# Kernel tuning notes

Hardware: AMD Instinct MI355X
Metric: run time of the kernel (lower is better)

The kernel has to match this reference:

```python
import jax, jax.numpy as jnp
import numpy as np
import math

B, S, D = 4, 2048, 1024
H, DH = 16, 64  # num_heads, head dim (hardcoded 64 in module)


def setup_inputs() -> dict:
    key = jax.random.key(0)
    ks = jax.random.split(key, 5)
    scale = 0.02
    return {
        "x": jax.random.normal(ks[0], (B, S, D), dtype=jnp.float32),
        "W_Q": jax.random.normal(ks[1], (D, H * DH), dtype=jnp.float32) * scale,
        "W_K": jax.random.normal(ks[2], (D, H * DH), dtype=jnp.float32) * scale,
        "W_V": jax.random.normal(ks[3], (D, H * DH), dtype=jnp.float32) * scale,
        "W_O": jax.random.normal(ks[4], (H * DH, D), dtype=jnp.float32) * scale,
        "ln_gamma": jnp.ones((D,), dtype=jnp.float32),
        "ln_beta": jnp.zeros((D,), dtype=jnp.float32),
    }


def reference(x, W_Q, W_K, W_V, W_O, ln_gamma, ln_beta):
    # QKV projections (bias=False Linear: x @ W)
    q = (x @ W_Q).reshape(B, S, H, DH).transpose(0, 2, 1, 3)  # [B,H,S,DH]
    k = (x @ W_K).reshape(B, S, H, DH).transpose(0, 2, 1, 3)
    v = (x @ W_V).reshape(B, S, H, DH).transpose(0, 2, 1, 3)

    # scaled scores with causal mask (upper triangle, diag=1 -> -1e7)
    scores = jnp.einsum("bhsd,bhtd->bhst", q, k) / math.sqrt(DH)  # [B,H,S,S]
    causal = jnp.triu(jnp.ones((S, S), dtype=bool), k=1)
    scores = jnp.where(causal, jnp.float32(-1e7), scores)
    attn = jax.nn.softmax(scores, axis=-1)
    ctx = jnp.einsum("bhst,bhtd->bhsd", attn, v)  # [B,H,S,DH]

    # merge heads, output proj, residual, LayerNorm
    out = ctx.transpose(0, 2, 1, 3).reshape(B, S, H * DH) @ W_O + x
    mu = jnp.mean(out, axis=-1, keepdims=True)
    var = jnp.mean((out - mu) ** 2, axis=-1, keepdims=True)
    out = (out - mu) * jax.lax.rsqrt(var + 1e-5) * ln_gamma + ln_beta
    return out
```

## Files before the change

### kernel.cpp

```cpp
#include <hip/hip_runtime.h>
#include <hip/hip_bf16.h>
#include <cstdint>
#include <cstddef>

#define S_ 2048
#define D_ 1024
#define H_ 16
#define DH_ 64
#define M_ 8192

using bf16 = __bf16;
using bf16x4 = __attribute__((ext_vector_type(4))) __bf16;
using bf16x8 = __attribute__((ext_vector_type(8))) __bf16;
using f32x4 = __attribute__((ext_vector_type(4))) float;
using s16x4 = __attribute__((ext_vector_type(4))) short;

__device__ __forceinline__ void g2lds16(const bf16* g, bf16* l) {
  __builtin_amdgcn_global_load_lds(
      (const __attribute__((address_space(1))) void*)g,
      (__attribute__((address_space(3))) void*)l, 16, 0, 0);
}

__device__ __forceinline__ f32x4 mfma16(bf16x4 a, bf16x4 b, f32x4 c) {
#if __has_builtin(__builtin_amdgcn_mfma_f32_16x16x16_bf16)
  return __builtin_amdgcn_mfma_f32_16x16x16_bf16(a, b, c, 0, 0, 0);
#elif __has_builtin(__builtin_amdgcn_mfma_f32_16x16x16bf16_1k)
  return __builtin_amdgcn_mfma_f32_16x16x16bf16_1k(
      __builtin_bit_cast(s16x4, a), __builtin_bit_cast(s16x4, b), c, 0, 0, 0);
#else
  f32x4 d;
  asm("v_mfma_f32_16x16x16_bf16 %0, %1, %2, %3"
      : "=v"(d)
      : "v"(a), "v"(b), "v"(c));
  return d;
#endif
}

__global__ __launch_bounds__(256) void cvt_all_kernel(
    const float* __restrict__ x, const float* __restrict__ w0,
    const float* __restrict__ w1, const float* __restrict__ w2,
    const float* __restrict__ w3, bf16* __restrict__ xb,
    bf16* __restrict__ o0, bf16* __restrict__ o1, bf16* __restrict__ o2,
    bf16* __restrict__ o3) {
  __shared__ float tile[32][33];
  int bx = blockIdx.x;
  int tid = threadIdx.x;
  if (bx < 4096) {
    size_t i = ((size_t)bx * 256 + tid) * 8;
    float4 a = *(const float4*)(x + i);
    float4 b = *(const float4*)(x + i + 4);
    bf16x8 o;
    o[0] = (bf16)a.x; o[1] = (bf16)a.y; o[2] = (bf16)a.z; o[3] = (bf16)a.w;
    o[4] = (bf16)b.x; o[5] = (bf16)b.y; o[6] = (bf16)b.z; o[7] = (bf16)b.w;
    *(bf16x8*)(xb + i) = o;
    return;
  }
  int wb = bx - 4096;
  int wsel = wb >> 10; wb &= 1023;
  const float* W; bf16* O;
  switch (wsel) {
    case 0: W = w0; O = o0; break;
    case 1: W = w1; O = o1; break;
    case 2: W = w2; O = o2; break;
    default: W = w3; O = o3; break;
  }
  int n0 = (wb & 31) * 32;
  int k0 = (wb >> 5) * 32;
#pragma unroll
  for (int i = 0; i < 4; ++i) {
    int e = tid + i * 256; int rr = e >> 5, cc = e & 31;
    tile[rr][cc] = W[(size_t)(k0 + rr) * 1024 + n0 + cc];
  }
  __syncthreads();
#pragma unroll
  for (int i = 0; i < 4; ++i) {
    int e = tid + i * 256; int rr = e >> 5, cc = e & 31;
    O[(size_t)(n0 + rr) * 1024 + k0 + cc] = (bf16)tile[cc][rr];
  }
}

__global__ __launch_bounds__(512, 4) void gemmA_kernel(
    const bf16* __restrict__ A, const bf16* __restrict__ Bt0,
    const bf16* __restrict__ Bt1, const bf16* __restrict__ Bt2,
    bf16* __restrict__ Qo, bf16* __restrict__ Ko, bf16* __restrict__ Vto) {
  extern __shared__ float4 smem4[];
  bf16* smem = (bf16*)smem4;

  const int wg = ((int)blockIdx.x & 7) * 96 + ((int)blockIdx.x >> 3);
  const int bn = wg % 12, bm = wg / 12;
  const int wsel = bn >> 2;
  const bf16* Bt = (wsel == 0) ? Bt0 : (wsel == 1 ? Bt1 : Bt2);
  const int n0full = (bn & 3) * 256;

  const int tid = threadIdx.x;
  const int wave = tid >> 6, lane = tid & 63;
  const int quad = lane >> 4, r = lane & 15;
  const int wm = (wave >> 2) * 64, wn = (wave & 3) * 64;

  const int lrow = lane >> 2;
  const int lcol = ((lane & 3) ^ ((lrow >> 1) & 3)) * 8;
  const int am = bm * 128 + wave * 16 + lrow;
  const bf16* pA = A + (size_t)am * 1024 + lcol;
  const int bnr = n0full + wave * 16 + lrow;
  const bf16* pB1 = Bt + (size_t)bnr * 1024 + lcol;
  const bf16* pB2 = Bt + (size_t)(bnr + 128) * 1024 + lcol;

  const int oA = wave * 512;
  const int oB1 = 4096 + wave * 512;
  const int oB2 = 8192 + wave * 512;

  auto stage = [&](bf16* base) {
    g2lds16(pA, base + oA); pA += 32;
    g2lds16(pB1, base + oB1); pB1 += 32;
    g2lds16(pB2, base + oB2); pB2 += 32;
  };

  f32x4 acc[4][4];
  const f32x4 zero = {0.f, 0.f, 0.f, 0.f};
#pragma unroll
  for (int i = 0; i < 4; ++i)
#pragma unroll
    for (int j = 0; j < 4; ++j) acc[i][j] = zero;

  const int x0 = (quad ^ ((r >> 1) & 3)) * 8;
  const int raB = (wm + r) * 32;
  const int rbB = (wn + r) * 32;

  auto phase = [&](const bf16* buf) {
    const bf16* bA = buf;
    const bf16* bB = buf + 4096;
    bf16x8 af[4], bg[4];
#pragma unroll
    for (int i = 0; i < 4; ++i)
      af[i] = *(const bf16x8*)(bA + raB + i * 512 + x0);
#pragma unroll
    for (int j = 0; j < 4; ++j)
      bg[j] = *(const bf16x8*)(bB + rbB + j * 512 + x0);
    __builtin_amdgcn_s_setprio(1);
#pragma unroll
    for (int i = 0; i < 4; ++i)
#pragma unroll
      for (int j = 0; j < 4; ++j)
        acc[i][j] = __builtin_amdgcn_mfma_f32_16x16x32_bf16(af[i], bg[j],
                                                            acc[i][j], 0, 0, 0);
    __builtin_amdgcn_s_setprio(0);
  };

  bf16* b0 = smem;
  bf16* b1 = smem + 12288;
  bf16* b2 = smem + 24576;

  stage(b0);
  stage(b1);

#pragma unroll 1
  for (int kt = 0; kt < 30; kt += 3) {
    asm volatile("s_waitcnt vmcnt(3)\n\ts_barrier" ::: "memory");
    stage(b2);
    phase(b0);
    asm volatile("s_waitcnt vmcnt(3)\n\ts_barrier" ::: "memory");
    stage(b0);
    phase(b1);
    asm volatile("s_waitcnt vmcnt(3)\n\ts_barrier" ::: "memory");
    stage(b1);
    phase(b2);
  }
  asm volatile("s_waitcnt vmcnt(3)\n\ts_barrier" ::: "memory");
  phase(b0);
  asm volatile("s_waitcnt vmcnt(0)\n\ts_barrier" ::: "memory");
  phase(b1);

  const int mB = bm * 128 + wm + quad * 4;
  if (wsel < 2) {
    bf16* dst = (wsel == 0) ? Qo : Ko;
#pragma unroll
    for (int i = 0; i < 4; ++i) {
#pragma unroll
      for (int j = 0; j < 4; ++j) {
        int n = n0full + wn + j * 16 + r;
        int h = n >> 6, dh = n & 63;
#pragma unroll
        for (int g = 0; g < 4; ++g) {
          int m = mB + i * 16 + g;
          int b = m >> 11, s = m & 2047;
          dst[((size_t)(b * H_ + h) * S_ + s) * DH_ + dh] = (bf16)acc[i][j][g];
        }
      }
    }
  } else {
#pragma unroll
    for (int i = 0; i < 4; ++i) {
      int m = mB + i * 16;
      int b = m >> 11, s = m & 2047;
#pragma unroll
      for (int j = 0; j < 4; ++j) {
        int n = n0full + wn + j * 16 + r;
        int h = n >> 6, dh = n & 63;
        bf16x4 pk;
#pragma unroll
        for (int g = 0; g < 4; ++g) pk[g] = (bf16)acc[i][j][g];
        *(bf16x4*)(Vto + ((size_t)(b * H_ + h) * DH_ + dh) * S_ + s) = pk;
      }
    }
  }
}

__global__ __launch_bounds__(512, 4) void gemmB_kernel(
    const bf16* __restrict__ A, const bf16* __restrict__ Bt0,
    bf16* __restrict__ Qo) {
  extern __shared__ float4 smem4[];
  bf16* smem = (bf16*)smem4;

  const int wg = ((int)blockIdx.x & 7) * 32 + ((int)blockIdx.x >> 3);
  const int bn = wg % 4, bm = wg / 4;
  const bf16* Bt = Bt0;
  const int n0full = bn * 256;

  const int tid = threadIdx.x;
  const int wave = tid >> 6, lane = tid & 63;
  const int quad = lane >> 4, r = lane & 15;
  const int wm = (wave >> 2) * 64, wn = (wave & 3) * 64;

  const int lrow = lane >> 2;
  const int lcol = ((lane & 3) ^ ((lrow >> 1) & 3)) * 8;
  const int am = bm * 128 + wave * 16 + lrow;
  const bf16* pA = A + (size_t)(am >> 11) * (16 * (size_t)S_ * DH_) +
                   (size_t)(am & 2047) * 64 + lcol;
  const int bnr = n0full + wave * 16 + lrow;
  const bf16* pB1 = Bt + (size_t)bnr * 1024 + lcol;
  const bf16* pB2 = Bt + (size_t)(bnr + 128) * 1024 + lcol;
  constexpr ptrdiff_t dSum = (ptrdiff_t)S_ * DH_;
  ptrdiff_t dTog = 32;

  const int oA = wave * 512;
  const int oB1 = 4096 + wave * 512;
  const int oB2 = 8192 + wave * 512;

  auto stage = [&](bf16* base) {
    g2lds16(pA, base + oA);
    g2lds16(pB1, base + oB1);
    g2lds16(pB2, base + oB2);
    pA += dTog; dTog = dSum - dTog;
    pB1 += 32; pB2 += 32;
  };

  f32x4 acc[4][4];
  const f32x4 zero = {0.f, 0.f, 0.f, 0.f};
#pragma unroll
  for (int i = 0; i < 4; ++i)
#pragma unroll
    for (int j = 0; j < 4; ++j) acc[i][j] = zero;

  const int x0 = (quad ^ ((r >> 1) & 3)) * 8;
  const int raB = (wm + r) * 32;
  const int rbB = (wn + r) * 32;

  auto phase = [&](const bf16* buf) {
    const bf16* bA = buf;
    const bf16* bB = buf + 4096;
    bf16x8 af[4], bg[4];
#pragma unroll
    for (int i = 0; i < 4; ++i)
      af[i] = *(const bf16x8*)(bA + raB + i * 512 + x0);
#pragma unroll
    for (int j = 0; j < 4; ++j)
      bg[j] = *(const bf16x8*)(bB + rbB + j * 512 + x0);
    __builtin_amdgcn_s_setprio(1);
#pragma unroll
    for (int i = 0; i < 4; ++i)
#pragma unroll
      for (int j = 0; j < 4; ++j)
        acc[i][j] = __builtin_amdgcn_mfma_f32_16x16x32_bf16(af[i], bg[j],
                                                            acc[i][j], 0, 0, 0);
    __builtin_amdgcn_s_setprio(0);
  };

  bf16* b0 = smem;
  bf16* b1 = smem + 12288;
  bf16* b2 = smem + 24576;

  stage(b0);
  stage(b1);

#pragma unroll 1
  for (int kt = 0; kt < 30; kt += 3) {
    asm volatile("s_waitcnt vmcnt(3)\n\ts_barrier" ::: "memory");
    stage(b2);
    phase(b0);
    asm volatile("s_waitcnt vmcnt(3)\n\ts_barrier" ::: "memory");
    stage(b0);
    phase(b1);
    asm volatile("s_waitcnt vmcnt(3)\n\ts_barrier" ::: "memory");
    stage(b1);
    phase(b2);
  }
  asm volatile("s_waitcnt vmcnt(3)\n\ts_barrier" ::: "memory");
  phase(b0);
  asm volatile("s_waitcnt vmcnt(0)\n\ts_barrier" ::: "memory");
  phase(b1);

  const int mB = bm * 128 + wm + quad * 4;
#pragma unroll
  for (int i = 0; i < 4; ++i) {
#pragma unroll
    for (int j = 0; j < 4; ++j) {
      int n = n0full + wn + j * 16 + r;
#pragma unroll
      for (int g = 0; g < 4; ++g) {
        int m = mB + i * 16 + g;
        Qo[(size_t)m * 1024 + n] = (bf16)acc[i][j][g];
      }
    }
  }
}

__global__ __launch_bounds__(512, 4) void attn_kernel(const bf16* __restrict__ Qb,
                                                      const bf16* __restrict__ Kb,
                                                      const bf16* __restrict__ Vtb,
                                                      bf16* __restrict__ ctx) {
  __shared__ __align__(16) bf16 smK[2][2][64 * 64];
  __shared__ __align__(16) bf16 smV[2][2][64 * 64];
  const int bx = blockIdx.x;
  const int bh = bx & 63;
  const int i256 = (bx < 256) ? (7 - (bx >> 6)) : ((bx - 256) >> 6);
  const bf16* Qh = Qb + (size_t)bh * S_ * DH_;
  const bf16* Kh = Kb + (size_t)bh * S_ * DH_;
  const bf16* Vh = Vtb + (size_t)bh * DH_ * S_;
  bf16* Ch = ctx + (size_t)bh * S_ * DH_;
  const int tid = threadIdx.x, wave = tid >> 6, lane = tid & 63;
  const int quad = lane >> 4, r = lane & 15;
  const int r7 = r & 7;
  const int wrow = wave * 8 + (lane >> 3);
  const int gcol = ((lane & 7) ^ (lane >> 3)) * 8;
  const f32x4 zero = {0.f, 0.f, 0.f, 0.f};
  const int xk0 = (quad ^ r7) * 8, xk1 = ((quad + 4) ^ r7) * 8;

  const int q0w = i256 * 256 + wave * 32;
  const int numkt = 4 * i256 + 4;
  const int NU = numkt >> 1;
  const int lastkt = q0w >> 6;

  bf16x8 qf[2][2];
  const float qsc = 0.125f * 1.44269504f;
#pragma unroll
  for (int qg = 0; qg < 2; ++qg)
#pragma unroll
    for (int hh = 0; hh < 2; ++hh) {
      bf16x8 q = *(const bf16x8*)(Qh + (size_t)(q0w + qg * 16 + r) * DH_ +
                                  hh * 32 + quad * 8);
#pragma unroll
      for (int i = 0; i < 8; ++i) q[i] = (bf16)((float)q[i] * qsc);
      qf[qg][hh] = q;
    }

  f32x4 lacc[2] = {zero, zero};
  f32x4 oacc[2][4];
#pragma unroll
  for (int qg = 0; qg < 2; ++qg)
#pragma unroll
    for (int tn = 0; tn < 4; ++tn) oacc[qg][tn] = zero;

  auto STAGE = [&](int u, int b) {
#pragma unroll
    for (int sub = 0; sub < 2; ++sub) {
      const int kt = 2 * u + sub;
      g2lds16(Kh + (size_t)(kt * 64 + wrow) * DH_ + gcol,
              &smK[b][sub][wave * 512]);
      g2lds16(Vh + (size_t)wrow * S_ + kt * 64 + gcol,
              &smV[b][sub][wave * 512]);
    }
  };

  STAGE(0, 0);
  asm volatile("s_waitcnt vmcnt(0)\n\ts_barrier" ::: "memory");

#pragma unroll 1
  for (int u = 0; u < NU; ++u) {
    const int b = u & 1;
    if (u + 1 < NU) STAGE(u + 1, b ^ 1);
#pragma unroll
    for (int sub = 0; sub < 2; ++sub) {
      const int kt = 2 * u + sub;
      if (kt <= lastkt) {
        const int kv0 = kt * 64;
        const bf16* kb = &smK[b][sub][0];
        const bf16* vb = &smV[b][sub][0];

        f32x4 s[2][4];
#pragma unroll
        for (int t = 0; t < 4; ++t) {
          bf16x8 kf0 = *(const bf16x8*)(kb + (t * 16 + r) * 64 + xk0);
          bf16x8 kf1 = *(const bf16x8*)(kb + (t * 16 + r) * 64 + xk1);
#pragma unroll
          for (int qg = 0; qg < 2; ++qg) {
            f32x4 z = __builtin_amdgcn_mfma_f32_16x16x32_bf16(kf0, qf[qg][0],
                                                              zero, 0, 0, 0);
            s[qg][t] = __builtin_amdgcn_mfma_f32_16x16x32_bf16(kf1, qf[qg][1],
                                                               z, 0, 0, 0);
          }
        }
        if (kt == lastkt) {
#pragma unroll
          for (int qg = 0; qg < 2; ++qg) {
            const int q = q0w + qg * 16 + r;
#pragma unroll
            for (int t = 0; t < 4; ++t) {
              const int kv = kv0 + t * 16 + quad * 4;
#pragma unroll
              for (int g = 0; g < 4; ++g)
                if (kv + g > q) s[qg][t][g] = -1e30f;
            }
          }
        }
#pragma unroll
        for (int t = 0; t < 4; ++t) {
          bf16x4 pa[2];
#pragma unroll
          for (int qg = 0; qg < 2; ++qg) {
#pragma unroll
            for (int g = 0; g < 4; ++g)
              s[qg][t][g] = __builtin_amdgcn_exp2f(s[qg][t][g]);
            lacc[qg] += s[qg][t];
            bf16x4 pk;
#pragma unroll
            for (int g = 0; g < 4; ++g) pk[g] = (bf16)s[qg][t][g];
            pa[qg] = pk;
          }
#pragma unroll
          for (int tn = 0; tn < 4; ++tn) {
            bf16x4 vf = *(const bf16x4*)(
                vb + (tn * 16 + r) * 64 +
                ((2 * t + (quad >> 1)) ^ r7) * 8 + (quad & 1) * 4);
            oacc[0][tn] = mfma16(pa[0], vf, oacc[0][tn]);
            oacc[1][tn] = mfma16(pa[1], vf, oacc[1][tn]);
          }
        }
      }
    }
    asm volatile("s_waitcnt vmcnt(0) lgkmcnt(0)\n\ts_barrier" ::: "memory");
  }

#pragma unroll
  for (int qg = 0; qg < 2; ++qg) {
    float rs = (lacc[qg][0] + lacc[qg][1]) + (lacc[qg][2] + lacc[qg][3]);
    rs += __shfl_xor(rs, 16, 64);
    rs += __shfl_xor(rs, 32, 64);
    const float inv = 1.f / rs;
    f32x4 ib;
#pragma unroll
    for (int g = 0; g < 4; ++g) ib[g] = __shfl(inv, quad * 4 + g, 64);
#pragma unroll
    for (int tn = 0; tn < 4; ++tn) {
      f32x4 ov = oacc[qg][tn] * ib;
#pragma unroll
      for (int g = 0; g < 4; ++g)
        Ch[(size_t)(q0w + qg * 16 + quad * 4 + g) * DH_ + tn * 16 + r] =
            (bf16)ov[g];
    }
  }
}

__global__ __launch_bounds__(256) void ln_kernel(float* __restrict__ out,
                                                 const bf16* __restrict__ pb,
                                                 const bf16* __restrict__ xb,
                                                 const float* __restrict__ gamma,
                                                 const float* __restrict__ beta) {
  __shared__ float red[8];
  size_t row = blockIdx.x;
  int tid = threadIdx.x;
  bf16x4 xv = *(const bf16x4*)(xb + row * 1024 + tid * 4);
  bf16x4 pv = *(const bf16x4*)(pb + row * 1024 + tid * 4);
  float v0 = (float)xv[0] + (float)pv[0];
  float v1 = (float)xv[1] + (float)pv[1];
  float v2 = (float)xv[2] + (float)pv[2];
  float v3 = (float)xv[3] + (float)pv[3];
  float s1 = v0 + v1 + v2 + v3;
  float s2 = v0 * v0 + v1 * v1 + v2 * v2 + v3 * v3;
#pragma unroll
  for (int o = 1; o < 64; o <<= 1) {
    s1 += __shfl_xor(s1, o, 64);
    s2 += __shfl_xor(s2, o, 64);
  }
  int wave = tid >> 6, lane = tid & 63;
  if (lane == 0) { red[wave] = s1; red[4 + wave] = s2; }
  __syncthreads();
  s1 = red[0] + red[1] + red[2] + red[3];
  s2 = red[4] + red[5] + red[6] + red[7];
  float mean = s1 * (1.f / 1024.f);
  float var = s2 * (1.f / 1024.f) - mean * mean;
  float rstd = rsqrtf(var + 1e-5f);
  float4 g = ((const float4*)gamma)[tid];
  float4 b = ((const float4*)beta)[tid];
  float4 o;
  o.x = (v0 - mean) * rstd * g.x + b.x;
  o.y = (v1 - mean) * rstd * g.y + b.y;
  o.z = (v2 - mean) * rstd * g.z + b.z;
  o.w = (v3 - mean) * rstd * g.w + b.w;
  ((float4*)(out + row * 1024))[tid] = o;
}

extern "C" void kernel_launch(void* const* d_in, const int* in_sizes, int n_in,
                              void* d_out, int out_size, void* d_ws,
                              size_t ws_size, hipStream_t stream) {
  (void)in_sizes; (void)n_in; (void)out_size; (void)ws_size;
  const float* x  = (const float*)d_in[0];
  const float* WQ = (const float*)d_in[1];
  const float* WK = (const float*)d_in[2];
  const float* WV = (const float*)d_in[3];
  const float* WO = (const float*)d_in[4];
  const float* gamma = (const float*)d_in[5];
  const float* beta  = (const float*)d_in[6];
  float* out = (float*)d_out;

  bf16* ws = (bf16*)d_ws;
  const size_t MD = (size_t)M_ * D_;
  const size_t WW = (size_t)D_ * D_;
  bf16* xb   = ws;
  bf16* wqt  = xb + MD;
  bf16* wkt  = wqt + WW;
  bf16* wvt  = wkt + WW;
  bf16* wot  = wvt + WW;
  bf16* Qb   = wot + WW;
  bf16* Kb   = Qb + MD;
  bf16* Vtb  = Kb + MD;
  bf16* ctxb = Vtb + MD;
  bf16* projb = Qb;

  constexpr int GEMM_LDS = 3 * 24 * 1024;
  static bool s_attr = false;
  if (!s_attr) {
    s_attr = true;
    (void)hipFuncSetAttribute(reinterpret_cast<const void*>(gemmA_kernel),
                              hipFuncAttributeMaxDynamicSharedMemorySize,
                              GEMM_LDS);
    (void)hipFuncSetAttribute(reinterpret_cast<const void*>(gemmB_kernel),
                              hipFuncAttributeMaxDynamicSharedMemorySize,
                              GEMM_LDS);
  }

  cvt_all_kernel<<<dim3(8192), dim3(256), 0, stream>>>(
      x, WQ, WK, WV, WO, xb, wqt, wkt, wvt, wot);
  gemmA_kernel<<<dim3(768), dim3(512), GEMM_LDS, stream>>>(
      xb, wqt, wkt, wvt, Qb, Kb, Vtb);
  attn_kernel<<<dim3(512), dim3(512), 0, stream>>>(Qb, Kb, Vtb, ctxb);
  gemmB_kernel<<<dim3(256), dim3(512), GEMM_LDS, stream>>>(
      ctxb, wot, projb);
  ln_kernel<<<dim3(8192), dim3(256), 0, stream>>>(out, projb, xb, gamma, beta);
}
```

Measured before the change: 238.4 us.

## Switch QKV GEMM from triple to double buffering to raise occupancy

The QKV projection GEMM moves from a three-buffer LDS pipeline to a two-buffer ping-pong. Each iteration now waits for all outstanding loads and LDS ops before the barrier. LDS per block drops from 72KB to 48KB and the launch-bounds occupancy hint rises from 4 to 6, so more blocks can be resident per CU. In exchange, each stage gets less prefetch depth, since every iteration stalls on the full vmcnt(0) before computing, which may expose global-load latency.

```diff
diff --git a/kernel.cpp b/kernel.cpp
--- a/kernel.cpp
+++ b/kernel.cpp
@@ -79,7 +79,7 @@
   }
 }
 
-__global__ __launch_bounds__(512, 4) void gemmA_kernel(
+__global__ __launch_bounds__(512, 6) void gemmA_kernel(
     const bf16* __restrict__ A, const bf16* __restrict__ Bt0,
     const bf16* __restrict__ Bt1, const bf16* __restrict__ Bt2,
     bf16* __restrict__ Qo, bf16* __restrict__ Ko, bf16* __restrict__ Vto) {
@@ -146,29 +146,16 @@
     __builtin_amdgcn_s_setprio(0);
   };
 
-  bf16* b0 = smem;
-  bf16* b1 = smem + 12288;
-  bf16* b2 = smem + 24576;
-
-  stage(b0);
-  stage(b1);
+  bf16* bufs[2] = {smem, smem + 12288};
+
+  stage(bufs[0]);
 
 #pragma unroll 1
-  for (int kt = 0; kt < 30; kt += 3) {
-    asm volatile("s_waitcnt vmcnt(3)\n\ts_barrier" ::: "memory");
-    stage(b2);
-    phase(b0);
-    asm volatile("s_waitcnt vmcnt(3)\n\ts_barrier" ::: "memory");
-    stage(b0);
-    phase(b1);
-    asm volatile("s_waitcnt vmcnt(3)\n\ts_barrier" ::: "memory");
-    stage(b1);
-    phase(b2);
-  }
-  asm volatile("s_waitcnt vmcnt(3)\n\ts_barrier" ::: "memory");
-  phase(b0);
-  asm volatile("s_waitcnt vmcnt(0)\n\ts_barrier" ::: "memory");
-  phase(b1);
+  for (int kt = 0; kt < 32; ++kt) {
+    asm volatile("s_waitcnt vmcnt(0) lgkmcnt(0)\n\ts_barrier" ::: "memory");
+    if (kt + 1 < 32) stage(bufs[(kt + 1) & 1]);
+    phase(bufs[kt & 1]);
+  }
 
   const int mB = bm * 128 + wm + quad * 4;
   if (wsel < 2) {
@@ -526,24 +513,25 @@
   bf16* ctxb = Vtb + MD;
   bf16* projb = Qb;
 
-  constexpr int GEMM_LDS = 3 * 24 * 1024;
+  constexpr int GEMMA_LDS = 2 * 24 * 1024;
+  constexpr int GEMMB_LDS = 3 * 24 * 1024;
   static bool s_attr = false;
   if (!s_attr) {
     s_attr = true;
     (void)hipFuncSetAttribute(reinterpret_cast<const void*>(gemmA_kernel),
                               hipFuncAttributeMaxDynamicSharedMemorySize,
-                              GEMM_LDS);
+                              GEMMA_LDS);
     (void)hipFuncSetAttribute(reinterpret_cast<const void*>(gemmB_kernel),
                               hipFuncAttributeMaxDynamicSharedMemorySize,
-                              GEMM_LDS);
+                              GEMMB_LDS);
   }
 
   cvt_all_kernel<<<dim3(8192), dim3(256), 0, stream>>>(
       x, WQ, WK, WV, WO, xb, wqt, wkt, wvt, wot);
-  gemmA_kernel<<<dim3(768), dim3(512), GEMM_LDS, stream>>>(
+  gemmA_kernel<<<dim3(768), dim3(512), GEMMA_LDS, stream>>>(
       xb, wqt, wkt, wvt, Qb, Kb, Vtb);
   attn_kernel<<<dim3(512), dim3(512), 0, stream>>>(Qb, Kb, Vtb, ctxb);
-  gemmB_kernel<<<dim3(256), dim3(512), GEMM_LDS, stream>>>(
+  gemmB_kernel<<<dim3(256), dim3(512), GEMMB_LDS, stream>>>(
       ctxb, wot, projb);
   ln_kernel<<<dim3(8192), dim3(256), 0, stream>>>(out, projb, xb, gamma, beta);
 }
```

Result: slower. 688.3 us (+188.7%).
